# Kernel optimization log

Measured on AMD Instinct MI355X. Metric: run time of the kernel, lower is better.

The kernel has to match this reference:

```python
import jax, jax.numpy as jnp
import numpy as np

LN_EPS = 1e-5


def layer_norm(x, g, b):
    m = jnp.mean(x, axis=-1, keepdims=True)
    v = jnp.mean(jnp.square(x - m), axis=-1, keepdims=True)
    return (x - m) * jax.lax.rsqrt(v + LN_EPS) * g + b


def sym_norm(A):
    # D^{-1/2} (A + I) D^{-1/2}
    N = A.shape[0]
    Ah = A + jnp.eye(N, dtype=A.dtype)
    d = jnp.sum(Ah, axis=-1)
    dinv = jax.lax.rsqrt(jnp.maximum(d, 1e-12))
    return Ah * dinv[:, None] * dinv[None, :]


def gru_layer(xs, Wih, Whh, bih, bhh):
    # xs: (BN, T, Din) -> ys: (BN, T, H). PyTorch GRU cell math.
    BN, T, _ = xs.shape
    H = Whh.shape[1]
    x_proj = xs @ Wih.T + bih  # (BN, T, 3H), precompute input projections

    def step(h, xp):
        hp = h @ Whh.T + bhh
        xr, xz, xn = jnp.split(xp, 3, axis=-1)
        hr, hz, hn = jnp.split(hp, 3, axis=-1)
        r = jax.nn.sigmoid(xr + hr)
        z = jax.nn.sigmoid(xz + hz)
        n = jnp.tanh(xn + r * hn)
        h_new = (1.0 - z) * n + z * h
        return h_new, h_new

    h0 = jnp.zeros((BN, H), xs.dtype)
    _, ys = jax.lax.scan(step, h0, jnp.swapaxes(x_proj, 0, 1))
    return jnp.swapaxes(ys, 0, 1)


def amscf_forward(x, A, FSP, DSP,
                  E1, E2, fus_W, fus_b, fus_v, beta1, beta2,
                  gcn_W1, gcn_b1, ln1_g, ln1_b, gcn_W2, gcn_b2, ln2_g, ln2_b,
                  gru_Wih0, gru_Whh0, gru_bih0, gru_bhh0,
                  gru_Wih1, gru_Whh1, gru_bih1, gru_bhh1,
                  att_w, fc1_W, fc1_b, fc2_W, fc2_b):
    B, T, N, _ = x.shape
    Hor = fc2_W.shape[0]

    # ImprovedAdjacency: blend A with adaptive node-embedding adjacency
    Aadp = jax.nn.softmax(jax.nn.relu(E1 @ E2.T), axis=-1)
    IA = 0.5 * A + 0.5 * Aadp

    # fuse_with_A with learned gates
    w1 = jax.nn.sigmoid(beta1)
    w2 = jax.nn.sigmoid(beta2)
    C1 = w1 * A + (1.0 - w1) * FSP
    C2 = w2 * A + (1.0 - w2) * DSP

    # TransposeAttentionFusion: graph-level attention over the 3 candidate graphs
    Gs = jnp.stack([IA, C1, C2], axis=0)  # (3, N, N)
    sc = jnp.mean(jnp.tanh(Gs @ fus_W.T + fus_b) @ fus_v, axis=-1)  # (3,)
    alpha = jax.nn.softmax(sc)
    MG = jnp.einsum('k,knm->nm', alpha, Gs)

    S_hat = sym_norm(MG)  # (N, N)

    # TwoLayerGCN over all (B, T) at once: act(LN(S X W1)) -> LN(S h W2)
    xf = x.reshape(B * T, N, 1)
    h = jnp.einsum('mn,bnc->bmc', S_hat, xf) @ gcn_W1 + gcn_b1
    h = jax.nn.relu(layer_norm(h, ln1_g, ln1_b))
    g = jnp.einsum('mn,bnc->bmc', S_hat, h) @ gcn_W2 + gcn_b2
    g = layer_norm(g, ln2_g, ln2_b)  # (B*T, N, C)

    C = g.shape[-1]
    # Faithful to original: raw view of (B, T, N, C) into (B*N, T, C)
    H_seq = g.reshape(B, T, N, C).reshape(B * N, T, C)

    out = gru_layer(H_seq, gru_Wih0, gru_Whh0, gru_bih0, gru_bhh0)
    out = gru_layer(out, gru_Wih1, gru_Whh1, gru_bih1, gru_bhh1)  # (BN, T, Hg)

    # SoftAttentionPooling over time
    score = out @ att_w  # (BN, T)
    att = jax.nn.softmax(score, axis=1)
    ctx = jnp.einsum('bt,bth->bh', att, out)

    hfc = jax.nn.gelu(ctx @ fc1_W.T + fc1_b)
    dlt = hfc @ fc2_W.T + fc2_b  # (BN, Hor); dropout is identity at eval
    return jnp.transpose(dlt.reshape(B, N, Hor), (0, 2, 1))  # (B, Hor, N)


def setup_inputs() -> dict:
    B, T, N, Hor = 32, 12, 1000, 12
    Cin, Ch, Cout, Hg, Da, De = 1, 96, 96, 192, 32, 10
    key = jax.random.key(0)
    ks = jax.random.split(key, 32)
    f32 = jnp.float32

    def nrm(k, shape, scale):
        return jax.random.normal(k, shape, dtype=f32) * scale

    inp = {
        'x': jax.random.normal(ks[0], (B, T, N, Cin), dtype=f32),
        'A': jax.random.uniform(ks[1], (N, N), dtype=f32),
        'FSP': jax.random.uniform(ks[2], (N, N), dtype=f32),
        'DSP': jax.random.uniform(ks[3], (N, N), dtype=f32),
        'E1': nrm(ks[4], (N, De), 0.1),
        'E2': nrm(ks[5], (N, De), 0.1),
        'fus_W': nrm(ks[6], (Da, N), 1.0 / np.sqrt(N)),
        'fus_b': jnp.zeros((Da,), f32),
        'fus_v': nrm(ks[7], (Da,), 1.0 / np.sqrt(Da)),
        'beta1': jnp.float32(0.5),
        'beta2': jnp.float32(0.5),
        'gcn_W1': nrm(ks[8], (Cin, Ch), 1.0 / np.sqrt(Cin)),
        'gcn_b1': jnp.zeros((Ch,), f32),
        'ln1_g': jnp.ones((Ch,), f32),
        'ln1_b': jnp.zeros((Ch,), f32),
        'gcn_W2': nrm(ks[9], (Ch, Cout), 1.0 / np.sqrt(Ch)),
        'gcn_b2': jnp.zeros((Cout,), f32),
        'ln2_g': jnp.ones((Cout,), f32),
        'ln2_b': jnp.zeros((Cout,), f32),
        'gru_Wih0': nrm(ks[10], (3 * Hg, Cout), 1.0 / np.sqrt(Hg)),
        'gru_Whh0': nrm(ks[11], (3 * Hg, Hg), 1.0 / np.sqrt(Hg)),
        'gru_bih0': jnp.zeros((3 * Hg,), f32),
        'gru_bhh0': jnp.zeros((3 * Hg,), f32),
        'gru_Wih1': nrm(ks[12], (3 * Hg, Hg), 1.0 / np.sqrt(Hg)),
        'gru_Whh1': nrm(ks[13], (3 * Hg, Hg), 1.0 / np.sqrt(Hg)),
        'gru_bih1': jnp.zeros((3 * Hg,), f32),
        'gru_bhh1': jnp.zeros((3 * Hg,), f32),
        'att_w': nrm(ks[14], (Hg,), 1.0 / np.sqrt(Hg)),
        'fc1_W': nrm(ks[15], (Hg, Hg), 1.0 / np.sqrt(Hg)),
        'fc1_b': jnp.zeros((Hg,), f32),
        'fc2_W': nrm(ks[16], (Hor, Hg), 1.0 / np.sqrt(Hg)),
        'fc2_b': jnp.zeros((Hor,), f32),
    }
    return inp


def reference(x, A, FSP, DSP, E1, E2, fus_W, fus_b, fus_v, beta1, beta2,
              gcn_W1, gcn_b1, ln1_g, ln1_b, gcn_W2, gcn_b2, ln2_g, ln2_b,
              gru_Wih0, gru_Whh0, gru_bih0, gru_bhh0,
              gru_Wih1, gru_Whh1, gru_bih1, gru_bhh1,
              att_w, fc1_W, fc1_b, fc2_W, fc2_b):
    return amscf_forward(x, A, FSP, DSP, E1, E2, fus_W, fus_b, fus_v, beta1, beta2,
                         gcn_W1, gcn_b1, ln1_g, ln1_b, gcn_W2, gcn_b2, ln2_g, ln2_b,
                         gru_Wih0, gru_Whh0, gru_bih0, gru_bhh0,
                         gru_Wih1, gru_Whh1, gru_bih1, gru_bhh1,
                         att_w, fc1_W, fc1_b, fc2_W, fc2_b)
```

## Files before the change

kernel.cpp:

```cpp
#include <hip/hip_runtime.h>

typedef unsigned short u16;
typedef unsigned int u32;
typedef __attribute__((ext_vector_type(8))) short short8;
typedef __attribute__((ext_vector_type(4))) float float4v;

#define DEV static __device__ __forceinline__

DEV float bf2f(u16 u) { u32 x = ((u32)u) << 16; float f; __builtin_memcpy(&f, &x, 4); return f; }
DEV u16 f2bf(float f) {
  u32 u; __builtin_memcpy(&u, &f, 4);
  u = (u + 0x7fffu + ((u >> 16) & 1u)) >> 16;
  return (u16)u;
}
DEV float sigm(float x) { return 1.f / (1.f + __expf(-x)); }

DEV void gl16(const u16* g, u16* l) {
  __builtin_amdgcn_global_load_lds(
      (const __attribute__((address_space(1))) void*)g,
      (__attribute__((address_space(3))) void*)l, 16, 0, 0);
}

template <int OMODE>
__launch_bounds__(256)
__global__ void gemm_nt(const u16* __restrict__ A, int lda,
                        const u16* __restrict__ B, int ldb,
                        void* __restrict__ Cp, int ldc,
                        int M, int N, int K,
                        const float* __restrict__ bias)
{
  constexpr int PK = 40;
  __shared__ u16 As[128 * PK];
  __shared__ u16 Bs[64 * PK];

  const int tid  = threadIdx.x;
  const int m0   = blockIdx.y * 128;
  const int n0   = blockIdx.x * 64;
  const int wid  = tid >> 6;
  const int lane = tid & 63;
  const int l15  = lane & 15;
  const int quad = lane >> 4;
  const int wm   = (wid >> 1) * 64;
  const int wn   = (wid & 1) * 32;

  float4v acc[4][2];
  const float4v fz = {0.f, 0.f, 0.f, 0.f};
#pragma unroll
  for (int i = 0; i < 4; i++)
#pragma unroll
    for (int j = 0; j < 2; j++) acc[i][j] = fz;

  const int arow = tid >> 2;
  const int akc  = tid & 3;

  const int kt_count = (K + 31) / 32;
  for (int kt = 0; kt < kt_count; ++kt) {
    const int k0 = kt * 32 + akc * 8;
    const bool kok = (k0 < K);
    uint4 av0 = make_uint4(0, 0, 0, 0), av1 = av0, bv = av0;
    int ra = m0 + arow;
    if (kok && ra < M)        av0 = *(const uint4*)(A + (size_t)ra * lda + k0);
    if (kok && ra + 64 < M)   av1 = *(const uint4*)(A + (size_t)(ra + 64) * lda + k0);
    int rb = n0 + arow;
    if (kok && rb < N)        bv  = *(const uint4*)(B + (size_t)rb * ldb + k0);

    __syncthreads();
    *(uint4*)&As[arow * PK + akc * 8]        = av0;
    *(uint4*)&As[(arow + 64) * PK + akc * 8] = av1;
    *(uint4*)&Bs[arow * PK + akc * 8]        = bv;
    __syncthreads();

    short8 af[4], bfr[2];
#pragma unroll
    for (int i = 0; i < 4; i++)
      af[i] = *(const short8*)&As[(wm + i * 16 + l15) * PK + quad * 8];
#pragma unroll
    for (int j = 0; j < 2; j++)
      bfr[j] = *(const short8*)&Bs[(wn + j * 16 + l15) * PK + quad * 8];
#pragma unroll
    for (int i = 0; i < 4; i++)
#pragma unroll
      for (int j = 0; j < 2; j++)
        acc[i][j] = __builtin_amdgcn_mfma_f32_16x16x32_bf16(af[i], bfr[j], acc[i][j], 0, 0, 0);
  }

#pragma unroll
  for (int i = 0; i < 4; i++)
#pragma unroll
    for (int j = 0; j < 2; j++)
#pragma unroll
      for (int e = 0; e < 4; e++) {
        int r = m0 + wm + i * 16 + quad * 4 + e;
        int c = n0 + wn + j * 16 + l15;
        if (r < M && c < N) {
          float v = acc[i][j][e];
          if (OMODE == 0) ((float*)Cp)[(size_t)r * ldc + c] = v;
          else {
            float a = v + bias[c];
            float t = tanhf(0.7978845608028654f * (a + 0.044715f * a * a * a));
            ((float*)Cp)[(size_t)r * ldc + c] = 0.5f * a * (1.f + t);
          }
        }
      }
}

__launch_bounds__(256)
__global__ void k_bigemm(const u16* __restrict__ A,
                         const u16* __restrict__ B,
                         const float* __restrict__ b2, const float* __restrict__ g2,
                         const float* __restrict__ be2,
                         u16* __restrict__ Gg)
{
  __shared__ u16 As[128 * 64];
  __shared__ u16 Bs[96 * 64];
  __shared__ float stats[2][2][128];

  const int tid  = threadIdx.x;
  const int bid  = blockIdx.x;
  const int xcd  = bid & 7;
  const int jj   = bid >> 3;
  const int m0   = (jj & 7) * 128;
  const int rt   = xcd + 8 * (jj >> 3);

  const int wid  = tid >> 6;
  const int lane = tid & 63;
  const int l15  = lane & 15;
  const int quad = lane >> 4;
  const int wm   = (wid >> 1) * 64;
  const int wn   = (wid & 1) * 48;
  const int wni  = wid & 1;

  const int srow8 = lane >> 3;
  const int sw8   = ((lane & 7) ^ srow8) * 8;

  const u16* abase = A + (size_t)(m0 + wid * 8 + srow8) * 1024 + sw8;
  const u16* bbase = B + (size_t)(rt * 96 + wid * 8 + srow8) * 1024 + sw8;

  float4v acc[4][3];
  const float4v fz = {0.f, 0.f, 0.f, 0.f};
#pragma unroll
  for (int i = 0; i < 4; i++)
#pragma unroll
    for (int j = 0; j < 3; j++) acc[i][j] = fz;

  for (int kt = 0; kt < 16; ++kt) {
    const int ko = kt * 64;
#pragma unroll
    for (int c = 0; c < 4; c++)
      gl16(abase + (size_t)c * 32 * 1024 + ko, &As[(c * 32 + wid * 8) * 64]);
#pragma unroll
    for (int c = 0; c < 3; c++)
      gl16(bbase + (size_t)c * 32 * 1024 + ko, &Bs[(c * 32 + wid * 8) * 64]);
    __syncthreads();
#pragma unroll
    for (int k32 = 0; k32 < 2; k32++) {
      const int swr = ((quad + 4 * k32) ^ (l15 & 7)) * 8;
      short8 af[4], bf[3];
#pragma unroll
      for (int i = 0; i < 4; i++)
        af[i] = *(const short8*)&As[(wm + i * 16 + l15) * 64 + swr];
#pragma unroll
      for (int j = 0; j < 3; j++)
        bf[j] = *(const short8*)&Bs[(wn + j * 16 + l15) * 64 + swr];
#pragma unroll
      for (int i = 0; i < 4; i++)
#pragma unroll
        for (int j = 0; j < 3; j++)
          acc[i][j] = __builtin_amdgcn_mfma_f32_16x16x32_bf16(af[i], bf[j], acc[i][j], 0, 0, 0);
    }
    __syncthreads();
  }

  float b2v[3], g2v[3], bev[3];
#pragma unroll
  for (int j = 0; j < 3; j++) {
    int c = wn + j * 16 + l15;
    b2v[j] = b2[c]; g2v[j] = g2[c]; bev[j] = be2[c];
  }
#pragma unroll
  for (int i = 0; i < 4; i++)
#pragma unroll
    for (int e = 0; e < 4; e++) {
      float s = 0.f, ss = 0.f;
#pragma unroll
      for (int j = 0; j < 3; j++) {
        float v = acc[i][j][e] + b2v[j];
        acc[i][j][e] = v;
        s += v; ss += v * v;
      }
      s += __shfl_xor(s, 1); ss += __shfl_xor(ss, 1);
      s += __shfl_xor(s, 2); ss += __shfl_xor(ss, 2);
      s += __shfl_xor(s, 4); ss += __shfl_xor(ss, 4);
      s += __shfl_xor(s, 8); ss += __shfl_xor(ss, 8);
      if (l15 == 0) {
        int rl = wm + i * 16 + quad * 4 + e;
        stats[wni][0][rl] = s;
        stats[wni][1][rl] = ss;
      }
    }
  __syncthreads();
#pragma unroll
  for (int i = 0; i < 4; i++)
#pragma unroll
    for (int e = 0; e < 4; e++) {
      int rl = wm + i * 16 + quad * 4 + e;
      int m = m0 + rl;
      if (m < 1000) {
        float ts  = stats[0][0][rl] + stats[1][0][rl];
        float tss = stats[0][1][rl] + stats[1][1][rl];
        float mean = ts * (1.f / 96.f);
        float var  = tss * (1.f / 96.f) - mean * mean;
        float isd  = rsqrtf(var + 1e-5f);
#pragma unroll
        for (int j = 0; j < 3; j++) {
          int c = wn + j * 16 + l15;
          Gg[(size_t)rt * 96000 + (size_t)m * 96 + c] =
              f2bf((acc[i][j][e] - mean) * isd * g2v[j] + bev[j]);
        }
      }
    }
}

DEV void pool_fold(int m0, int c0, int pm,
                   const u16* __restrict__ Hpool,
                   const float* __restrict__ score_rd,
                   const float* __restrict__ Mrd, const float* __restrict__ Lrd,
                   float* __restrict__ Mwr, float* __restrict__ Lwr,
                   float* __restrict__ Nvp)
{
  const int tid = threadIdx.x;
#pragma unroll
  for (int k = 0; k < 16; k++) {
    int idx = k * 256 + tid;
    int ql = idx >> 5, cl = idx & 31;
    int q = m0 + ql, c = c0 + cl;
    size_t nidx = (size_t)q * 192 + c;
    float s = score_rd[q];
    float hnew = bf2f(Hpool[nidx]);
    float so, wnf, prev;
    if (pm == 1) { so = 0.f; wnf = 1.f; prev = 0.f; }
    else {
      float Mo = Mrd[q];
      float Mn = fmaxf(Mo, s);
      so = __expf(Mo - Mn); wnf = __expf(s - Mn);
      prev = Nvp[nidx];
    }
    Nvp[nidx] = prev * so + wnf * hnew;
  }
  if (c0 == 0 && tid < 128) {
    int q = m0 + tid;
    float s = score_rd[q];
    if (pm == 1) { Mwr[q] = s; Lwr[q] = 1.f; }
    else {
      float Mo = Mrd[q], Mn = fmaxf(Mo, s);
      Mwr[q] = Mn;
      Lwr[q] = Lrd[q] * __expf(Mo - Mn) + __expf(s - Mn);
    }
  }
}

template <int KX, bool POOL>
DEV void gru_tile(u16* As, u16* Bs,
                  int m0, int c0,
                  const u16* __restrict__ Xin, int ldx,
                  const u16* __restrict__ Win,
                  const u16* __restrict__ Hin,
                  const u16* __restrict__ Whh,
                  const float* __restrict__ bih, const float* __restrict__ bhh,
                  u16* __restrict__ Hout,
                  const float* __restrict__ att_w,
                  float* __restrict__ score_acc,
                  const u16* __restrict__ Hpool,
                  const float* __restrict__ score_rd,
                  const float* __restrict__ Mrd, const float* __restrict__ Lrd,
                  float* __restrict__ Mwr, float* __restrict__ Lwr,
                  float* __restrict__ Nvp,
                  int t0, int pm)
{
  const int tid  = threadIdx.x;
  const int wid  = tid >> 6;
  const int lane = tid & 63;
  const int l15  = lane & 15;
  const int quad = lane >> 4;
  const int wm   = wid * 32;

  if (!POOL && pm)
    pool_fold(m0, c0, pm, Hpool, score_rd, Mrd, Lrd, Mwr, Lwr, Nvp);

  const int srow8 = lane >> 3;
  const int sw8   = ((lane & 7) ^ srow8) * 8;
  const int srow4 = lane >> 2;
  const int sw4   = ((lane & 3) ^ ((lane >> 3) & 3)) * 8;

  float4v aR[2][2], aZ[2][2], aXN[2][2], aHN[2][2];
  const float4v fz = {0.f, 0.f, 0.f, 0.f};
#pragma unroll
  for (int i = 0; i < 2; i++)
#pragma unroll
    for (int j = 0; j < 2; j++) { aR[i][j] = fz; aZ[i][j] = fz; aXN[i][j] = fz; aHN[i][j] = fz; }

  if (KX == 96) {
    const u16* ax0 = Xin + (size_t)(m0 + wid * 16 + srow4) * ldx + sw4;
    const u16* ax1 = Xin + (size_t)(m0 + 64 + wid * 16 + srow4) * ldx + sw4;
    const int b0 = wid * 16 + srow4;
    const u16* bx0 = Win + (size_t)((b0 >> 5) * 192 + c0 + (b0 & 31)) * 96 + sw4;
    const int b1 = 64 + wid * 16 + srow4;
    const u16* bx1 = Win + (size_t)(384 + c0 + (b1 & 31)) * 96 + sw4;
    u16* asl0 = &As[(wid * 16) * 32];
    u16* asl1 = &As[(64 + wid * 16) * 32];
    u16* bsl0 = &Bs[(wid * 16) * 32];
    u16* bsl1 = &Bs[(64 + wid * 16) * 32];
    const int swa = (quad ^ ((l15 >> 1) & 3)) * 8;
#pragma unroll
    for (int kt = 0; kt < 3; ++kt) {
      const int ko = kt * 32;
      gl16(ax0 + ko, asl0); gl16(ax1 + ko, asl1);
      gl16(bx0 + ko, bsl0);
      if (wid < 2) gl16(bx1 + ko, bsl1);
      __syncthreads();
      short8 af[2], bR[2], bZ[2], bN[2];
#pragma unroll
      for (int i = 0; i < 2; i++)
        af[i] = *(const short8*)&As[(wm + i * 16 + l15) * 32 + swa];
#pragma unroll
      for (int j = 0; j < 2; j++) {
        bR[j] = *(const short8*)&Bs[(j * 16 + l15) * 32 + swa];
        bZ[j] = *(const short8*)&Bs[(32 + j * 16 + l15) * 32 + swa];
        bN[j] = *(const short8*)&Bs[(64 + j * 16 + l15) * 32 + swa];
      }
#pragma unroll
      for (int i = 0; i < 2; i++)
#pragma unroll
        for (int j = 0; j < 2; j++) {
          aR[i][j]  = __builtin_amdgcn_mfma_f32_16x16x32_bf16(af[i], bR[j], aR[i][j], 0, 0, 0);
          aZ[i][j]  = __builtin_amdgcn_mfma_f32_16x16x32_bf16(af[i], bZ[j], aZ[i][j], 0, 0, 0);
          aXN[i][j] = __builtin_amdgcn_mfma_f32_16x16x32_bf16(af[i], bN[j], aXN[i][j], 0, 0, 0);
        }
      __syncthreads();
    }
  } else {
    const u16* abase = Xin + (size_t)(m0 + wid * 8 + srow8) * 192 + sw8;
    const u16* bbase = Win + (size_t)(c0 + wid * 8 + srow8) * 192 + sw8;
#pragma unroll
    for (int kt = 0; kt < 3; ++kt) {
      const int ko = kt * 64;
#pragma unroll
      for (int c = 0; c < 4; c++)
        gl16(abase + (size_t)c * 32 * 192 + ko, &As[(c * 32 + wid * 8) * 64]);
#pragma unroll
      for (int c = 0; c < 3; c++)
        gl16(bbase + (size_t)c * 192 * 192 + ko, &Bs[(c * 32 + wid * 8) * 64]);
      __syncthreads();
#pragma unroll
      for (int k32 = 0; k32 < 2; k32++) {
        const int swr = ((quad + 4 * k32) ^ (l15 & 7)) * 8;
        short8 af[2], bR[2], bZ[2], bN[2];
#pragma unroll
        for (int i = 0; i < 2; i++)
          af[i] = *(const short8*)&As[(wm + i * 16 + l15) * 64 + swr];
#pragma unroll
        for (int j = 0; j < 2; j++) {
          bR[j] = *(const short8*)&Bs[(j * 16 + l15) * 64 + swr];
          bZ[j] = *(const short8*)&Bs[(32 + j * 16 + l15) * 64 + swr];
          bN[j] = *(const short8*)&Bs[(64 + j * 16 + l15) * 64 + swr];
        }
#pragma unroll
        for (int i = 0; i < 2; i++)
#pragma unroll
          for (int j = 0; j < 2; j++) {
            aR[i][j]  = __builtin_amdgcn_mfma_f32_16x16x32_bf16(af[i], bR[j], aR[i][j], 0, 0, 0);
            aZ[i][j]  = __builtin_amdgcn_mfma_f32_16x16x32_bf16(af[i], bZ[j], aZ[i][j], 0, 0, 0);
            aXN[i][j] = __builtin_amdgcn_mfma_f32_16x16x32_bf16(af[i], bN[j], aXN[i][j], 0, 0, 0);
          }
      }
      __syncthreads();
    }
  }
  if (!t0) {
    const u16* abase = Hin + (size_t)(m0 + wid * 8 + srow8) * 192 + sw8;
    const u16* bbase = Whh + (size_t)(c0 + wid * 8 + srow8) * 192 + sw8;
#pragma unroll
    for (int kt = 0; kt < 3; ++kt) {
      const int ko = kt * 64;
#pragma unroll
      for (int c = 0; c < 4; c++)
        gl16(abase + (size_t)c * 32 * 192 + ko, &As[(c * 32 + wid * 8) * 64]);
#pragma unroll
      for (int c = 0; c < 3; c++)
        gl16(bbase + (size_t)c * 192 * 192 + ko, &Bs[(c * 32 + wid * 8) * 64]);
      __syncthreads();
#pragma unroll
      for (int k32 = 0; k32 < 2; k32++) {
        const int swr = ((quad + 4 * k32) ^ (l15 & 7)) * 8;
        short8 af[2], bR[2], bZ[2], bN[2];
#pragma unroll
        for (int i = 0; i < 2; i++)
          af[i] = *(const short8*)&As[(wm + i * 16 + l15) * 64 + swr];
#pragma unroll
        for (int j = 0; j < 2; j++) {
          bR[j] = *(const short8*)&Bs[(j * 16 + l15) * 64 + swr];
          bZ[j] = *(const short8*)&Bs[(32 + j * 16 + l15) * 64 + swr];
          bN[j] = *(const short8*)&Bs[(64 + j * 16 + l15) * 64 + swr];
        }
#pragma unroll
        for (int i = 0; i < 2; i++)
#pragma unroll
          for (int j = 0; j < 2; j++) {
            aR[i][j]  = __builtin_amdgcn_mfma_f32_16x16x32_bf16(af[i], bR[j], aR[i][j], 0, 0, 0);
            aZ[i][j]  = __builtin_amdgcn_mfma_f32_16x16x32_bf16(af[i], bZ[j], aZ[i][j], 0, 0, 0);
            aHN[i][j] = __builtin_amdgcn_mfma_f32_16x16x32_bf16(af[i], bN[j], aHN[i][j], 0, 0, 0);
          }
      }
      __syncthreads();
    }
  }

  float ps[2][4];
  if (POOL) {
#pragma unroll
    for (int i = 0; i < 2; i++)
#pragma unroll
      for (int e = 0; e < 4; e++) ps[i][e] = 0.f;
  }
#pragma unroll
  for (int j = 0; j < 2; ++j) {
    const int c = c0 + j * 16 + l15;
    const float brz = bih[c] + bhh[c];
    const float bzz = bih[192 + c] + bhh[192 + c];
    const float bxn = bih[384 + c];
    const float bhn = bhh[384 + c];
    const float aw  = POOL ? att_w[c] : 0.f;
#pragma unroll
    for (int i = 0; i < 2; ++i)
#pragma unroll
      for (int e = 0; e < 4; ++e) {
        const int row = m0 + wm + i * 16 + quad * 4 + e;
        float rg  = sigm(aR[i][j][e] + brz);
        float zg  = sigm(aZ[i][j][e] + bzz);
        float hnv = bhn + (t0 ? 0.f : aHN[i][j][e]);
        float ng  = tanhf(aXN[i][j][e] + bxn + rg * hnv);
        float hold = t0 ? 0.f : bf2f(Hin[(size_t)row * 192 + c]);
        float hnew = (1.f - zg) * ng + zg * hold;
        Hout[(size_t)row * 192 + c] = f2bf(hnew);
        if (POOL) ps[i][e] += hnew * aw;
      }
  }
  if (POOL) {
#pragma unroll
    for (int i = 0; i < 2; ++i)
#pragma unroll
      for (int e = 0; e < 4; ++e) {
        float v = ps[i][e];
        v += __shfl_xor(v, 1); v += __shfl_xor(v, 2);
        v += __shfl_xor(v, 4); v += __shfl_xor(v, 8);
        if (l15 == 0) atomicAdd(&score_acc[m0 + wm + i * 16 + quad * 4 + e], v);
      }
  }
}

struct GruArgs {
  const u16 *Gg, *Wih0, *Whh0, *Wih1, *Whh1;
  const float *bih0, *bhh0, *bih1, *bhh1, *att_w;
  u16 *h0[2];
  u16 *h1[3];
  float *M[2], *L[2], *s[3];
  float* Nv;
};

__launch_bounds__(256)
__global__ void k_gru2(GruArgs a, int u)
{
  __shared__ u16 As[128 * 64];
  __shared__ u16 Bs[96 * 64];
  const int m0 = blockIdx.y * 128;

  if (blockIdx.x < 6) {
    const int c0 = blockIdx.x * 32;
    const int pm = (u < 2) ? 0 : (u == 2 ? 1 : 2);
    if (u > 11) {
      if (pm)
        pool_fold(m0, c0, pm, a.h1[(u + 1) % 3], a.s[(u + 1) % 3],
                  a.M[(u + 1) & 1], a.L[(u + 1) & 1], a.M[u & 1], a.L[u & 1], a.Nv);
      return;
    }
    if (c0 == 0 && threadIdx.x < 128) a.s[u % 3][m0 + threadIdx.x] = 0.f;
    gru_tile<96, false>(As, Bs, m0, c0,
        a.Gg + u * 96, 1152, a.Wih0, a.h0[u & 1], a.Whh0, a.bih0, a.bhh0, a.h0[(u & 1) ^ 1],
        nullptr, nullptr,
        a.h1[(u + 1) % 3], a.s[(u + 1) % 3],
        a.M[(u + 1) & 1], a.L[(u + 1) & 1],
        a.M[u & 1], a.L[u & 1],
        a.Nv, u == 0, pm);
  } else {
    if (u < 1) return;
    const int t = u - 1;
    const int c0 = (blockIdx.x - 6) * 32;
    gru_tile<192, true>(As, Bs, m0, c0,
        a.h0[u & 1], 192, a.Wih1, a.h1[(u + 1) % 3], a.Whh1, a.bih1, a.bhh1, a.h1[t % 3],
        a.att_w, a.s[t % 3],
        nullptr, nullptr, nullptr, nullptr, nullptr, nullptr, nullptr,
        t == 0, 0);
  }
}

__launch_bounds__(256)
__global__ void k_h2gemm(const float* __restrict__ yt, const float4* __restrict__ cwpk,
                         const u16* __restrict__ W2s, const float* __restrict__ consts,
                         u16* __restrict__ h2t)
{
  constexpr int PK = 40;
  __shared__ u16 As[128 * PK];
  __shared__ u16 Bs[96 * PK];
  __shared__ u16 Ts[96 * 136];

  const int tid  = threadIdx.x;
  const int m0   = blockIdx.x * 128;
  const int wid  = tid >> 6;
  const int lane = tid & 63;
  const int l15  = lane & 15;
  const int quad = lane >> 4;
  const int wm   = (wid >> 1) * 64;
  const int wn   = (wid & 1) * 48;

  const float P = consts[0], Q = consts[1], VW = consts[2], CWB = consts[3], VB = consts[4];

  const int arow = tid >> 2;
  const int akc  = tid & 3;

  float yv[2], mu[2], iv[2];
#pragma unroll
  for (int rr = 0; rr < 2; rr++) {
    int i = m0 + arow + rr * 64;
    int r = i / 1000, n = i - r * 1000;
    float y = yt[n * 384 + r];
    yv[rr] = y;
    mu[rr] = y * P + Q;
    iv[rr] = rsqrtf(y * y * VW + 2.f * y * CWB + VB + 1e-5f);
  }

  float4v acc[4][3];
  const float4v fz = {0.f, 0.f, 0.f, 0.f};
#pragma unroll
  for (int i = 0; i < 4; i++)
#pragma unroll
    for (int j = 0; j < 3; j++) acc[i][j] = fz;

  uint4 asave[2][3];
  const bool has2 = (arow < 32);

  for (int kt = 0; kt < 6; ++kt) {
    const int k0 = kt * 32 + akc * 8;
    uint4 av[2];
    if (kt < 3) {
#pragma unroll
      for (int rr = 0; rr < 2; rr++) {
        u16 hb[8];
#pragma unroll
        for (int e = 0; e < 8; e++) {
          float4 cw = cwpk[k0 + e];
          float t = yv[rr] * cw.x + cw.y - mu[rr];
          float h = fmaxf(t * iv[rr] * cw.z + cw.w, 0.f);
          hb[e] = f2bf(h);
        }
        __builtin_memcpy(&av[rr], hb, 16);
        asave[rr][kt] = av[rr];
      }
    } else {
      av[0] = asave[0][kt - 3];
      av[1] = asave[1][kt - 3];
    }
    uint4 bv0 = *(const uint4*)(W2s + (size_t)arow * 192 + k0);
    uint4 bv1 = make_uint4(0, 0, 0, 0);
    if (has2) bv1 = *(const uint4*)(W2s + (size_t)(arow + 64) * 192 + k0);

    __syncthreads();
    *(uint4*)&As[arow * PK + akc * 8]        = av[0];
    *(uint4*)&As[(arow + 64) * PK + akc * 8] = av[1];
    *(uint4*)&Bs[arow * PK + akc * 8]        = bv0;
    if (has2) *(uint4*)&Bs[(arow + 64) * PK + akc * 8] = bv1;
    __syncthreads();

    short8 af[4], bfr[3];
#pragma unroll
    for (int i = 0; i < 4; i++)
      af[i] = *(const short8*)&As[(wm + i * 16 + l15) * PK + quad * 8];
#pragma unroll
    for (int j = 0; j < 3; j++)
      bfr[j] = *(const short8*)&Bs[(wn + j * 16 + l15) * PK + quad * 8];
#pragma unroll
    for (int i = 0; i < 4; i++)
#pragma unroll
      for (int j = 0; j < 3; j++)
        acc[i][j] = __builtin_amdgcn_mfma_f32_16x16x32_bf16(af[i], bfr[j], acc[i][j], 0, 0, 0);
  }

#pragma unroll
  for (int i = 0; i < 4; i++)
#pragma unroll
    for (int j = 0; j < 3; j++)
#pragma unroll
      for (int e = 0; e < 4; e++) {
        int rowl = wm + i * 16 + quad * 4 + e;
        int c2   = wn + j * 16 + l15;
        Ts[c2 * 136 + rowl] = f2bf(acc[i][j][e]);
      }
  __syncthreads();
#pragma unroll
  for (int u = tid; u < 1536; u += 256) {
    int c2 = u >> 4, ch = u & 15;
    int iidx0 = m0 + ch * 8;
    int r = iidx0 / 1000, n0 = iidx0 - r * 1000;
    *(uint4*)(h2t + (size_t)(r * 96 + c2) * 1024 + n0) = *(const uint4*)&Ts[c2 * 136 + ch * 8];
  }
}

__launch_bounds__(256)
__global__ void k_prep(const float* x, const float* fus_W,
                       const float* Wih0, const float* Whh0,
                       const float* Wih1, const float* Whh1,
                       const float* gcn_W1, const float* gcn_b1,
                       const float* gcn_W2, const float* ln1g, const float* ln1b,
                       const float* fc1W,
                       u16* xbf, u16* fusWbf, u16* Wih0b, u16* Whh0b, u16* Wih1b, u16* Whh1b,
                       u16* W2s, float4* cwpk, float* scp, u16* w1s, float* fusWT,
                       u16* h2t, float* s0, float* s1, float* s2, float* consts)
{
  long o = (long)blockIdx.x * 256 + threadIdx.x;
  if (o < 384000) xbf[o] = f2bf(x[o]);
  else if ((o -= 384000) < 32000) fusWbf[o] = f2bf(fus_W[o]);
  else if ((o -= 32000) < 55296)  Wih0b[o] = f2bf(Wih0[o]);
  else if ((o -= 55296) < 110592) Whh0b[o] = f2bf(Whh0[o]);
  else if ((o -= 110592) < 110592) Wih1b[o] = f2bf(Wih1[o]);
  else if ((o -= 110592) < 110592) Whh1b[o] = f2bf(Whh1[o]);
  else if ((o -= 110592) < 9216) {
    int c2 = (int)o / 96, c = (int)o - c2 * 96;
    float wv = gcn_W2[c * 96 + c2];
    u16 hi = f2bf(wv);
    u16 lo = f2bf(wv - bf2f(hi));
    W2s[c2 * 192 + c] = hi;
    W2s[c2 * 192 + 96 + c] = lo;
  }
  else if ((o -= 9216) < 96) {
    int c = (int)o;
    float4 cw;
    cw.x = gcn_W1[c]; cw.y = gcn_b1[c]; cw.z = ln1g[c]; cw.w = ln1b[c];
    cwpk[c] = cw;
  }
  else if ((o -= 96) < 3) scp[o] = 0.f;
  else if ((o -= 3) < 36864) {
    int n = (int)o / 192, k = (int)o - n * 192;
    float wv = fc1W[o];
    u16 hi = f2bf(wv);
    u16 lo = f2bf(wv - bf2f(hi));
    w1s[(size_t)n * 576 + k]       = hi;
    w1s[(size_t)n * 576 + 192 + k] = lo;
    w1s[(size_t)n * 576 + 384 + k] = hi;
  }
  else if ((o -= 36864) < 32000) {
    int m = (int)o >> 5, a = (int)o & 31;
    fusWT[o] = fus_W[a * 1000 + m];
  }
  else if ((o -= 32000) < 110592) {
    int row = (int)o / 3, p = (int)o - row * 3;
    *(uint4*)(h2t + (size_t)row * 1024 + 1000 + p * 8) = make_uint4(0, 0, 0, 0);
  }
  else if ((o -= 110592) < 96000) {
    if (o < 32000) s0[o] = 0.f;
    else if (o < 64000) s1[o - 32000] = 0.f;
    else s2[o - 64000] = 0.f;
  }
  if (blockIdx.x == 0 && threadIdx.x == 0) {
    float sw = 0, sb = 0, sww = 0, swb = 0, sbb = 0;
    for (int c = 0; c < 96; c++) {
      float wv = gcn_W1[c], b = gcn_b1[c];
      sw += wv; sb += b; sww += wv * wv; swb += wv * b; sbb += b * b;
    }
    float P = sw / 96.f, Q = sb / 96.f;
    consts[0] = P; consts[1] = Q;
    consts[2] = sww / 96.f - P * P;
    consts[3] = swb / 96.f - P * Q;
    consts[4] = sbb / 96.f - Q * Q;
  }
}

__launch_bounds__(256)
__global__ void k_adjrow(const float* __restrict__ A, const float* __restrict__ FSP,
                         const float* __restrict__ DSP, const float* __restrict__ E1,
                         const float* __restrict__ E2,
                         const float* beta1, const float* beta2,
                         const float* __restrict__ fusWT,
                         const float* __restrict__ fus_b, const float* __restrict__ fus_v,
                         u16* __restrict__ G, float* __restrict__ rowsums,
                         float* __restrict__ scp)
{
  __shared__ float z[1000];
  __shared__ float red[256];
  __shared__ float gk[3000];
  __shared__ float pred[768];
  __shared__ float vred[96];
  const int n = blockIdx.x, tid = threadIdx.x;

  float e1r[10];
#pragma unroll
  for (int d = 0; d < 10; d++) e1r[d] = E1[n * 10 + d];

  float lmax = -1e30f;
  for (int m = tid; m < 1000; m += 256) {
    float s = 0;
#pragma unroll
    for (int d = 0; d < 10; d++) s += e1r[d] * E2[m * 10 + d];
    s = fmaxf(s, 0.f);
    z[m] = s;
    lmax = fmaxf(lmax, s);
  }
  red[tid] = lmax; __syncthreads();
  for (int st = 128; st > 0; st >>= 1) { if (tid < st) red[tid] = fmaxf(red[tid], red[tid + st]); __syncthreads(); }
  const float mx = red[0]; __syncthreads();

  float lsum = 0;
  for (int m = tid; m < 1000; m += 256) { float e = __expf(z[m] - mx); z[m] = e; lsum += e; }
  red[tid] = lsum; __syncthreads();
  for (int st = 128; st > 0; st >>= 1) { if (tid < st) red[tid] += red[tid + st]; __syncthreads(); }
  const float inv = 1.f / red[0]; __syncthreads();

  const float w1 = sigm(beta1[0]);
  const float w2 = sigm(beta2[0]);
  float s0 = 0, s1 = 0, s2 = 0;
  for (int m = tid; m < 1000; m += 256) {
    float aadp = z[m] * inv;
    float a = A[n * 1000 + m], f = FSP[n * 1000 + m], dd = DSP[n * 1000 + m];
    float g0 = 0.5f * a + 0.5f * aadp;
    float g1 = w1 * a + (1.f - w1) * f;
    float g2 = w2 * a + (1.f - w2) * dd;
    G[0 * 1000000 + n * 1000 + m] = f2bf(g0);
    G[1 * 1000000 + n * 1000 + m] = f2bf(g1);
    G[2 * 1000000 + n * 1000 + m] = f2bf(g2);
    gk[m] = g0; gk[1000 + m] = g1; gk[2000 + m] = g2;
    s0 += g0; s1 += g1; s2 += g2;
  }
  red[tid] = s0; __syncthreads();
  for (int st = 128; st > 0; st >>= 1) { if (tid < st) red[tid] += red[tid + st]; __syncthreads(); }
  if (tid == 0) rowsums[n] = red[0];
  __syncthreads();
  red[tid] = s1; __syncthreads();
  for (int st = 128; st > 0; st >>= 1) { if (tid < st) red[tid] += red[tid + st]; __syncthreads(); }
  if (tid == 0) rowsums[1000 + n] = red[0];
  __syncthreads();
  red[tid] = s2; __syncthreads();
  for (int st = 128; st > 0; st >>= 1) { if (tid < st) red[tid] += red[tid + st]; __syncthreads(); }
  if (tid == 0) rowsums[2000 + n] = red[0];
  __syncthreads();

  const int a = tid & 31, grp = tid >> 5;
  float p0 = 0.f, p1 = 0.f, p2 = 0.f;
  for (int m = grp; m < 1000; m += 8) {
    float wv = fusWT[m * 32 + a];
    p0 += gk[m] * wv;
    p1 += gk[1000 + m] * wv;
    p2 += gk[2000 + m] * wv;
  }
  pred[0 * 256 + a * 8 + grp] = p0;
  pred[1 * 256 + a * 8 + grp] = p1;
  pred[2 * 256 + a * 8 + grp] = p2;
  __syncthreads();
  if (tid < 96) {
    int k = tid >> 5, aa = tid & 31;
    float P = 0.f;
#pragma unroll
    for (int g = 0; g < 8; g++) P += pred[k * 256 + aa * 8 + g];
    vred[k * 32 + aa] = tanhf(P + fus_b[aa]) * fus_v[aa];
  }
  __syncthreads();
  if (tid < 3) {
    float s = 0.f;
#pragma unroll
    for (int aa = 0; aa < 32; aa++) s += vred[tid * 32 + aa];
    atomicAdd(&scp[tid], s * 0.001f);
  }
}

__launch_bounds__(256)
__global__ void k_alpha(const float* sc, const float* rowsums, float* alpha_out, float* dinv)
{
  __shared__ float al[3];
  const int tid = threadIdx.x;
  if (tid == 0) {
    float m = fmaxf(sc[0], fmaxf(sc[1], sc[2]));
    float e0 = __expf(sc[0] - m), e1 = __expf(sc[1] - m), e2 = __expf(sc[2] - m);
    float inv = 1.f / (e0 + e1 + e2);
    al[0] = e0 * inv; al[1] = e1 * inv; al[2] = e2 * inv;
    alpha_out[0] = al[0]; alpha_out[1] = al[1]; alpha_out[2] = al[2];
  }
  __syncthreads();
  const float a0 = al[0], a1 = al[1], a2 = al[2];
  for (int n = tid; n < 1000; n += 256) {
    float d = a0 * rowsums[n] + a1 * rowsums[1000 + n] + a2 * rowsums[2000 + n] + 1.0f;
    dinv[n] = rsqrtf(fmaxf(d, 1e-12f));
  }
}

__launch_bounds__(256)
__global__ void k_shat(const u16* __restrict__ G, const float* alpha, const float* dinv,
                       u16* __restrict__ S)
{
  int idx = blockIdx.x * 256 + threadIdx.x;
  if (idx >= 1024000) return;
  int i = idx >> 10, j = idx & 1023;
  u16 val = 0;
  if (j < 1000) {
    const float a0 = alpha[0], a1 = alpha[1], a2 = alpha[2];
    int g = i * 1000 + j;
    float mg = a0 * bf2f(G[g]) + a1 * bf2f(G[1000000 + g]) + a2 * bf2f(G[2000000 + g]);
    if (i == j) mg += 1.0f;
    val = f2bf(mg * dinv[i] * dinv[j]);
  }
  S[(size_t)i * 1024 + j] = val;
}

__launch_bounds__(256)
__global__ void k_ctxsplit(const float* __restrict__ Nv, const u16* __restrict__ Hlast,
                           const float* __restrict__ score_rd,
                           const float* __restrict__ Mrd, const float* __restrict__ Lrd,
                           u16* __restrict__ ctxs)
{
  const int i = blockIdx.x * 256 + threadIdx.x;
  if (i >= 32000 * 192) return;
  const int q = i / 192, c = i - q * 192;
  const float s = score_rd[q];
  const float Mo = Mrd[q];
  const float Mn = fmaxf(Mo, s);
  const float so = __expf(Mo - Mn);
  const float wn = __expf(s - Mn);
  const float L = Lrd[q] * so + wn;
  float v = (Nv[i] * so + wn * bf2f(Hlast[i])) / L;
  u16 hi = f2bf(v);
  u16 lo = f2bf(v - bf2f(hi));
  u16* row = ctxs + (size_t)q * 576;
  row[c] = hi; row[192 + c] = hi; row[384 + c] = lo;
}

__launch_bounds__(192)
__global__ void k_fc2(const float* __restrict__ hfc, const float* __restrict__ fc2W,
                      const float* __restrict__ fc2b, float* __restrict__ out)
{
  __shared__ float w2S[12][193];
  __shared__ float hS[16][193];
  const int tid = threadIdx.x;
  const int q0 = blockIdx.x * 16;
  for (int idx = tid; idx < 12 * 192; idx += 192) {
    int o = idx / 192, k = idx - o * 192;
    w2S[o][k] = fc2W[idx];
  }
  for (int idx = tid; idx < 16 * 192; idx += 192) {
    int qq = idx / 192, k = idx - qq * 192;
    hS[qq][k] = hfc[(size_t)(q0 + qq) * 192 + k];
  }
  __syncthreads();
  const int qq = tid / 12, o = tid - qq * 12;
  float acc = fc2b[o];
#pragma unroll 8
  for (int k = 0; k < 192; k++) acc += hS[qq][k] * w2S[o][k];
  const int q = q0 + qq;
  const int b = q / 1000, node = q - b * 1000;
  out[(size_t)b * 12000 + o * 1000 + node] = acc;
}

extern "C" void kernel_launch(void* const* d_in, const int* in_sizes, int n_in,
                              void* d_out, int out_size, void* d_ws, size_t ws_size,
                              hipStream_t stream)
{
  const float* x     = (const float*)d_in[0];
  const float* A     = (const float*)d_in[1];
  const float* FSP   = (const float*)d_in[2];
  const float* DSP   = (const float*)d_in[3];
  const float* E1    = (const float*)d_in[4];
  const float* E2    = (const float*)d_in[5];
  const float* fus_W = (const float*)d_in[6];
  const float* fus_b = (const float*)d_in[7];
  const float* fus_v = (const float*)d_in[8];
  const float* beta1 = (const float*)d_in[9];
  const float* beta2 = (const float*)d_in[10];
  const float* gcn_W1= (const float*)d_in[11];
  const float* gcn_b1= (const float*)d_in[12];
  const float* ln1g  = (const float*)d_in[13];
  const float* ln1b  = (const float*)d_in[14];
  const float* gcn_W2= (const float*)d_in[15];
  const float* gcn_b2= (const float*)d_in[16];
  const float* ln2g  = (const float*)d_in[17];
  const float* ln2b  = (const float*)d_in[18];
  const float* Wih0  = (const float*)d_in[19];
  const float* Whh0  = (const float*)d_in[20];
  const float* bih0  = (const float*)d_in[21];
  const float* bhh0  = (const float*)d_in[22];
  const float* Wih1  = (const float*)d_in[23];
  const float* Whh1  = (const float*)d_in[24];
  const float* bih1  = (const float*)d_in[25];
  const float* bhh1  = (const float*)d_in[26];
  const float* att_w = (const float*)d_in[27];
  const float* fc1W  = (const float*)d_in[28];
  const float* fc1b  = (const float*)d_in[29];
  const float* fc2W  = (const float*)d_in[30];
  const float* fc2b  = (const float*)d_in[31];
  float* out = (float*)d_out;

  char* w = (char*)d_ws;
  auto alloc = [&](size_t bytes) -> char* {
    char* p = w;
    w += (bytes + 255) & ~(size_t)255;
    return p;
  };

  float* consts  = (float*)alloc(8 * 4);
  float* scp     = (float*)alloc(3 * 4);
  float* alphap  = (float*)alloc(3 * 4);
  float* rowsums = (float*)alloc(3000 * 4);
  float* dinvp   = (float*)alloc(1000 * 4);
  u16*   Gbuf    = (u16*)alloc((size_t)3000000 * 2);
  u16*   Sbf     = (u16*)alloc((size_t)1024 * 1024 * 2);
  u16*   xbf     = (u16*)alloc((size_t)384000 * 2);
  u16*   fusWbf  = (u16*)alloc((size_t)32000 * 2);
  u16*   Wih0b   = (u16*)alloc((size_t)55296 * 2);
  u16*   Whh0b   = (u16*)alloc((size_t)110592 * 2);
  u16*   Wih1b   = (u16*)alloc((size_t)110592 * 2);
  u16*   Whh1b   = (u16*)alloc((size_t)110592 * 2);
  u16*   w1s     = (u16*)alloc((size_t)192 * 576 * 2);
  u16*   W2s     = (u16*)alloc((size_t)96 * 192 * 2);
  float4* cwpk   = (float4*)alloc((size_t)96 * 16);
  float* fusWT   = (float*)alloc((size_t)32000 * 4);
  float* yt      = (float*)alloc((size_t)384000 * 4);
  u16*   h2t     = (u16*)alloc((size_t)36864 * 1024 * 2);
  u16*   Gg      = (u16*)alloc((size_t)36864000 * 2);
  float* Nv      = (float*)alloc((size_t)6144000 * 4);
  float* Mb0     = (float*)alloc((size_t)32000 * 4);
  float* Mb1     = (float*)alloc((size_t)32000 * 4);
  float* Lb0     = (float*)alloc((size_t)32000 * 4);
  float* Lb1     = (float*)alloc((size_t)32000 * 4);
  float* sc0     = (float*)alloc((size_t)32000 * 4);
  float* sc1     = (float*)alloc((size_t)32000 * 4);
  float* sc2     = (float*)alloc((size_t)32000 * 4);

  u16* h0s[2] = { h2t,                    h2t + (size_t)6144000 };
  u16* h1s[3] = { h2t + (size_t)12288000, h2t + (size_t)18432000, h2t + (size_t)24576000 };
  u16*   ctxs = h2t;
  float* hfc  = (float*)(h2t + (size_t)18432000);

  k_prep<<<4250, 256, 0, stream>>>(x, fus_W, Wih0, Whh0, Wih1, Whh1, gcn_W1, gcn_b1,
                                   gcn_W2, ln1g, ln1b, fc1W,
                                   xbf, fusWbf, Wih0b, Whh0b, Wih1b, Whh1b, W2s, cwpk,
                                   scp, w1s, fusWT, h2t, sc0, sc1, sc2, consts);
  k_adjrow<<<1000, 256, 0, stream>>>(A, FSP, DSP, E1, E2, beta1, beta2,
                                     fusWT, fus_b, fus_v, Gbuf, rowsums, scp);
  k_alpha<<<1, 256, 0, stream>>>(scp, rowsums, alphap, dinvp);
  k_shat<<<4000, 256, 0, stream>>>(Gbuf, alphap, dinvp, Sbf);
  gemm_nt<0><<<dim3(6, 8), 256, 0, stream>>>(Sbf, 1024, xbf, 1000, yt, 384, 1000, 384, 1000, nullptr);
  k_h2gemm<<<3000, 256, 0, stream>>>(yt, cwpk, W2s, consts, h2t);
  k_bigemm<<<3072, 256, 0, stream>>>(Sbf, h2t, gcn_b2, ln2g, ln2b, Gg);

  GruArgs ga;
  ga.Gg = Gg; ga.Wih0 = Wih0b; ga.Whh0 = Whh0b; ga.Wih1 = Wih1b; ga.Whh1 = Whh1b;
  ga.bih0 = bih0; ga.bhh0 = bhh0; ga.bih1 = bih1; ga.bhh1 = bhh1; ga.att_w = att_w;
  ga.h0[0] = h0s[0]; ga.h0[1] = h0s[1];
  ga.h1[0] = h1s[0]; ga.h1[1] = h1s[1]; ga.h1[2] = h1s[2];
  ga.M[0] = Mb0; ga.M[1] = Mb1; ga.L[0] = Lb0; ga.L[1] = Lb1;
  ga.s[0] = sc0; ga.s[1] = sc1; ga.s[2] = sc2;
  ga.Nv = Nv;
  for (int u = 0; u <= 12; ++u)
    k_gru2<<<dim3(12, 250), 256, 0, stream>>>(ga, u);

  k_ctxsplit<<<24000, 256, 0, stream>>>(Nv, h1s[2], sc2, Mb0, Lb0, ctxs);
  gemm_nt<3><<<dim3(3, 250), 256, 0, stream>>>(ctxs, 576, w1s, 576, hfc, 192, 32000, 192, 576, fc1b);
  k_fc2<<<2000, 192, 0, stream>>>(hfc, fc2W, fc2b, out);
}
```

Before: 1.425 ms.

## Widen bigemm N-tile to two slices per block and fold alpha into shat

The big S×H GEMM now covers two 96-column slices per block (192 columns), with each wave owning one full 96-wide slice. LayerNorm statistics can then be reduced inside the wave by shuffles alone, with no shared-memory stats exchange and no extra barrier. The grid is halved, so each loaded A tile is reused across twice as many columns, at the cost of more accumulator registers and possibly lower occupancy. Separately, the single-block alpha/dinv kernel is removed: each k_shat thread recomputes the softmax and both degree normalisers inline, saving one launch at the cost of redundant arithmetic.

```diff
diff --git a/kernel.cpp b/kernel.cpp
--- a/kernel.cpp
+++ b/kernel.cpp
@@ -112,36 +112,35 @@
                          u16* __restrict__ Gg)
 {
   __shared__ u16 As[128 * 64];
-  __shared__ u16 Bs[96 * 64];
-  __shared__ float stats[2][2][128];
+  __shared__ u16 Bs[192 * 64];
 
   const int tid  = threadIdx.x;
   const int bid  = blockIdx.x;
   const int xcd  = bid & 7;
   const int jj   = bid >> 3;
   const int m0   = (jj & 7) * 128;
-  const int rt   = xcd + 8 * (jj >> 3);
+  const int rt2  = xcd + 8 * (jj >> 3);
 
   const int wid  = tid >> 6;
   const int lane = tid & 63;
   const int l15  = lane & 15;
   const int quad = lane >> 4;
   const int wm   = (wid >> 1) * 64;
-  const int wn   = (wid & 1) * 48;
+  const int wn   = (wid & 1) * 96;
   const int wni  = wid & 1;
 
   const int srow8 = lane >> 3;
   const int sw8   = ((lane & 7) ^ srow8) * 8;
 
   const u16* abase = A + (size_t)(m0 + wid * 8 + srow8) * 1024 + sw8;
-  const u16* bbase = B + (size_t)(rt * 96 + wid * 8 + srow8) * 1024 + sw8;
-
-  float4v acc[4][3];
+  const u16* bbase = B + (size_t)(rt2 * 192 + wid * 8 + srow8) * 1024 + sw8;
+
+  float4v acc[4][6];
   const float4v fz = {0.f, 0.f, 0.f, 0.f};
 #pragma unroll
   for (int i = 0; i < 4; i++)
 #pragma unroll
-    for (int j = 0; j < 3; j++) acc[i][j] = fz;
+    for (int j = 0; j < 6; j++) acc[i][j] = fz;
 
   for (int kt = 0; kt < 16; ++kt) {
     const int ko = kt * 64;
@@ -149,33 +148,34 @@
     for (int c = 0; c < 4; c++)
       gl16(abase + (size_t)c * 32 * 1024 + ko, &As[(c * 32 + wid * 8) * 64]);
 #pragma unroll
-    for (int c = 0; c < 3; c++)
+    for (int c = 0; c < 6; c++)
       gl16(bbase + (size_t)c * 32 * 1024 + ko, &Bs[(c * 32 + wid * 8) * 64]);
     __syncthreads();
 #pragma unroll
     for (int k32 = 0; k32 < 2; k32++) {
       const int swr = ((quad + 4 * k32) ^ (l15 & 7)) * 8;
-      short8 af[4], bf[3];
+      short8 af[4], bf[6];
 #pragma unroll
       for (int i = 0; i < 4; i++)
         af[i] = *(const short8*)&As[(wm + i * 16 + l15) * 64 + swr];
 #pragma unroll
-      for (int j = 0; j < 3; j++)
+      for (int j = 0; j < 6; j++)
         bf[j] = *(const short8*)&Bs[(wn + j * 16 + l15) * 64 + swr];
 #pragma unroll
       for (int i = 0; i < 4; i++)
 #pragma unroll
-        for (int j = 0; j < 3; j++)
+        for (int j = 0; j < 6; j++)
           acc[i][j] = __builtin_amdgcn_mfma_f32_16x16x32_bf16(af[i], bf[j], acc[i][j], 0, 0, 0);
     }
     __syncthreads();
   }
 
-  float b2v[3], g2v[3], bev[3];
-#pragma unroll
-  for (int j = 0; j < 3; j++) {
-    int c = wn + j * 16 + l15;
-    b2v[j] = b2[c]; g2v[j] = g2[c]; bev[j] = be2[c];
+  const int rs = rt2 * 2 + wni;
+  float b2v[6], g2v[6], bev[6];
+#pragma unroll
+  for (int j = 0; j < 6; j++) {
+    int cc = j * 16 + l15;
+    b2v[j] = b2[cc]; g2v[j] = g2[cc]; bev[j] = be2[cc];
   }
 #pragma unroll
   for (int i = 0; i < 4; i++)
@@ -183,7 +183,7 @@
     for (int e = 0; e < 4; e++) {
       float s = 0.f, ss = 0.f;
 #pragma unroll
-      for (int j = 0; j < 3; j++) {
+      for (int j = 0; j < 6; j++) {
         float v = acc[i][j][e] + b2v[j];
         acc[i][j][e] = v;
         s += v; ss += v * v;
@@ -192,29 +192,15 @@
       s += __shfl_xor(s, 2); ss += __shfl_xor(ss, 2);
       s += __shfl_xor(s, 4); ss += __shfl_xor(ss, 4);
       s += __shfl_xor(s, 8); ss += __shfl_xor(ss, 8);
-      if (l15 == 0) {
-        int rl = wm + i * 16 + quad * 4 + e;
-        stats[wni][0][rl] = s;
-        stats[wni][1][rl] = ss;
-      }
-    }
-  __syncthreads();
-#pragma unroll
-  for (int i = 0; i < 4; i++)
-#pragma unroll
-    for (int e = 0; e < 4; e++) {
-      int rl = wm + i * 16 + quad * 4 + e;
-      int m = m0 + rl;
+      const int m = m0 + wm + i * 16 + quad * 4 + e;
       if (m < 1000) {
-        float ts  = stats[0][0][rl] + stats[1][0][rl];
-        float tss = stats[0][1][rl] + stats[1][1][rl];
-        float mean = ts * (1.f / 96.f);
-        float var  = tss * (1.f / 96.f) - mean * mean;
+        float mean = s * (1.f / 96.f);
+        float var  = ss * (1.f / 96.f) - mean * mean;
         float isd  = rsqrtf(var + 1e-5f);
 #pragma unroll
-        for (int j = 0; j < 3; j++) {
-          int c = wn + j * 16 + l15;
-          Gg[(size_t)rt * 96000 + (size_t)m * 96 + c] =
+        for (int j = 0; j < 6; j++) {
+          int cc = j * 16 + l15;
+          Gg[(size_t)rs * 96000 + (size_t)m * 96 + cc] =
               f2bf((acc[i][j][e] - mean) * isd * g2v[j] + bev[j]);
         }
       }
@@ -780,39 +766,25 @@
 }
 
 __launch_bounds__(256)
-__global__ void k_alpha(const float* sc, const float* rowsums, float* alpha_out, float* dinv)
-{
-  __shared__ float al[3];
-  const int tid = threadIdx.x;
-  if (tid == 0) {
-    float m = fmaxf(sc[0], fmaxf(sc[1], sc[2]));
-    float e0 = __expf(sc[0] - m), e1 = __expf(sc[1] - m), e2 = __expf(sc[2] - m);
-    float inv = 1.f / (e0 + e1 + e2);
-    al[0] = e0 * inv; al[1] = e1 * inv; al[2] = e2 * inv;
-    alpha_out[0] = al[0]; alpha_out[1] = al[1]; alpha_out[2] = al[2];
-  }
-  __syncthreads();
-  const float a0 = al[0], a1 = al[1], a2 = al[2];
-  for (int n = tid; n < 1000; n += 256) {
-    float d = a0 * rowsums[n] + a1 * rowsums[1000 + n] + a2 * rowsums[2000 + n] + 1.0f;
-    dinv[n] = rsqrtf(fmaxf(d, 1e-12f));
-  }
-}
-
-__launch_bounds__(256)
-__global__ void k_shat(const u16* __restrict__ G, const float* alpha, const float* dinv,
-                       u16* __restrict__ S)
+__global__ void k_shat(const u16* __restrict__ G, const float* __restrict__ scp,
+                       const float* __restrict__ rowsums, u16* __restrict__ S)
 {
   int idx = blockIdx.x * 256 + threadIdx.x;
   if (idx >= 1024000) return;
   int i = idx >> 10, j = idx & 1023;
   u16 val = 0;
+  const float sc0 = scp[0], sc1 = scp[1], sc2 = scp[2];
+  const float mm = fmaxf(sc0, fmaxf(sc1, sc2));
+  const float e0 = __expf(sc0 - mm), e1 = __expf(sc1 - mm), e2 = __expf(sc2 - mm);
+  const float inv = 1.f / (e0 + e1 + e2);
+  const float a0 = e0 * inv, a1 = e1 * inv, a2 = e2 * inv;
   if (j < 1000) {
-    const float a0 = alpha[0], a1 = alpha[1], a2 = alpha[2];
+    float di = rsqrtf(fmaxf(a0 * rowsums[i] + a1 * rowsums[1000 + i] + a2 * rowsums[2000 + i] + 1.0f, 1e-12f));
+    float dj = rsqrtf(fmaxf(a0 * rowsums[j] + a1 * rowsums[1000 + j] + a2 * rowsums[2000 + j] + 1.0f, 1e-12f));
     int g = i * 1000 + j;
     float mg = a0 * bf2f(G[g]) + a1 * bf2f(G[1000000 + g]) + a2 * bf2f(G[2000000 + g]);
     if (i == j) mg += 1.0f;
-    val = f2bf(mg * dinv[i] * dinv[j]);
+    val = f2bf(mg * di * dj);
   }
   S[(size_t)i * 1024 + j] = val;
 }
@@ -912,9 +884,7 @@
 
   float* consts  = (float*)alloc(8 * 4);
   float* scp     = (float*)alloc(3 * 4);
-  float* alphap  = (float*)alloc(3 * 4);
   float* rowsums = (float*)alloc(3000 * 4);
-  float* dinvp   = (float*)alloc(1000 * 4);
   u16*   Gbuf    = (u16*)alloc((size_t)3000000 * 2);
   u16*   Sbf     = (u16*)alloc((size_t)1024 * 1024 * 2);
   u16*   xbf     = (u16*)alloc((size_t)384000 * 2);
@@ -950,11 +920,10 @@
                                    scp, w1s, fusWT, h2t, sc0, sc1, sc2, consts);
   k_adjrow<<<1000, 256, 0, stream>>>(A, FSP, DSP, E1, E2, beta1, beta2,
                                      fusWT, fus_b, fus_v, Gbuf, rowsums, scp);
-  k_alpha<<<1, 256, 0, stream>>>(scp, rowsums, alphap, dinvp);
-  k_shat<<<4000, 256, 0, stream>>>(Gbuf, alphap, dinvp, Sbf);
+  k_shat<<<4000, 256, 0, stream>>>(Gbuf, scp, rowsums, Sbf);
   gemm_nt<0><<<dim3(6, 8), 256, 0, stream>>>(Sbf, 1024, xbf, 1000, yt, 384, 1000, 384, 1000, nullptr);
   k_h2gemm<<<3000, 256, 0, stream>>>(yt, cwpk, W2s, consts, h2t);
-  k_bigemm<<<3072, 256, 0, stream>>>(Sbf, h2t, gcn_b2, ln2g, ln2b, Gg);
+  k_bigemm<<<1536, 256, 0, stream>>>(Sbf, h2t, gcn_b2, ln2g, ln2b, Gg);
 
   GruArgs ga;
   ga.Gg = Gg; ga.Wih0 = Wih0b; ga.Whh0 = Whh0b; ga.Wih1 = Wih1b; ga.Whh1 = Whh1b;
```

Result: no change. 1.422 ms (-0.2%).
